# Performance work log

Hardware: AMD Instinct MI355X
Metric: run time of the kernel (lower is better)

Reference implementation:

```python
import jax, jax.numpy as jnp
import numpy as np

B_, DIM, HEADS, RES = 2, 288, 12, 32
# per-branch (D_sp, H_sp, W_sp) from idx permutation of split_size=[2,2,4]
WINS = ((2, 2, 4), (2, 2, 4), (2, 4, 2))
POS_DIM = ((DIM // 3) // 4) // 4  # = 6
HB = HEADS // 3  # heads per branch = 4


def _rel_tables(Dsp, Hsp, Wsp):
    d = np.arange(1 - Dsp, Dsp); h = np.arange(1 - Hsp, Hsp); w = np.arange(1 - Wsp, Wsp)
    biases = np.stack(np.meshgrid(d, h, w, indexing='ij')).reshape(3, -1).T.astype(np.float32)
    c = np.stack(np.meshgrid(np.arange(Dsp), np.arange(Hsp), np.arange(Wsp), indexing='ij')).reshape(3, -1)
    rel = (c[:, :, None] - c[:, None, :]).transpose(1, 2, 0).astype(np.int64)
    rel[..., 0] += Dsp - 1; rel[..., 1] += Hsp - 1; rel[..., 2] += Wsp - 1
    rel[..., 0] *= (2 * Hsp - 1) * (2 * Wsp - 1); rel[..., 1] *= 2 * Wsp - 1
    return biases, rel.sum(-1).astype(np.int32)


def _ln(x, g, b):
    m = x.mean(-1, keepdims=True)
    v = jnp.mean((x - m) ** 2, axis=-1, keepdims=True)
    return (x - m) * jax.lax.rsqrt(v + 1e-5) * g + b


def setup_inputs() -> dict:
    key = jax.random.key(0)
    ks = jax.random.split(key, 10)
    C, P, L = DIM, POS_DIM, RES ** 3
    s = 0.02
    x = jax.random.normal(ks[0], (B_, L, C), jnp.float32)
    w_qkv = jax.random.normal(ks[1], (C, 3 * C), jnp.float32) * s
    w_proj = jax.random.normal(ks[2], (C, C), jnp.float32) * s
    b_proj = jnp.zeros((C,), jnp.float32)
    conv_w = jax.random.normal(ks[3], (C, 1, 3, 3, 3), jnp.float32) * s  # depthwise OIDHW
    conv_b = jnp.zeros((C,), jnp.float32)
    pos_proj_w = jax.random.normal(ks[4], (3, 3, P), jnp.float32) * s
    pos_proj_b = jnp.zeros((3, P), jnp.float32)
    ln1_g = jnp.ones((3, P)); ln1_b = jnp.zeros((3, P))
    lin1_w = jax.random.normal(ks[5], (3, P, P), jnp.float32) * s; lin1_b = jnp.zeros((3, P))
    ln2_g = jnp.ones((3, P)); ln2_b = jnp.zeros((3, P))
    lin2_w = jax.random.normal(ks[6], (3, P, P), jnp.float32) * s; lin2_b = jnp.zeros((3, P))
    ln3_g = jnp.ones((3, P)); ln3_b = jnp.zeros((3, P))
    lin3_w = jax.random.normal(ks[7], (3, P, HB), jnp.float32) * s; lin3_b = jnp.zeros((3, HB))
    tabs = [_rel_tables(*w) for w in WINS]
    rpe_biases = jnp.asarray(np.stack([t[0] for t in tabs]))  # (3, 63, 3)
    rel_index = jnp.asarray(np.stack([t[1] for t in tabs]))   # (3, 16, 16)
    return {'x': x, 'D': RES, 'H': RES, 'W': RES, 'w_qkv': w_qkv, 'w_proj': w_proj,
            'b_proj': b_proj, 'conv_w': conv_w, 'conv_b': conv_b,
            'pos_proj_w': pos_proj_w, 'pos_proj_b': pos_proj_b,
            'ln1_g': ln1_g, 'ln1_b': ln1_b, 'lin1_w': lin1_w, 'lin1_b': lin1_b,
            'ln2_g': ln2_g, 'ln2_b': ln2_b, 'lin2_w': lin2_w, 'lin2_b': lin2_b,
            'ln3_g': ln3_g, 'ln3_b': ln3_b, 'lin3_w': lin3_w, 'lin3_b': lin3_b,
            'rpe_biases': rpe_biases, 'rel_index': rel_index}


def reference(x, D, H, W, w_qkv, w_proj, b_proj, conv_w, conv_b,
              pos_proj_w, pos_proj_b, ln1_g, ln1_b, lin1_w, lin1_b,
              ln2_g, ln2_b, lin2_w, lin2_b, ln3_g, ln3_b, lin3_w, lin3_b,
              rpe_biases, rel_index):
    B, L, C = x.shape
    C3 = C // 3
    hd = C3 // HB
    scale = hd ** -0.5
    qkv = (x @ w_qkv).reshape(B, L, 3, C).transpose(2, 0, 1, 3)  # (3, B, L, C)
    outs = []
    for bi, (Dsp, Hsp, Wsp) in enumerate(WINS):
        N = Dsp * Hsp * Wsp
        lo, hi = bi * C3, (bi + 1) * C3

        def to_win(t):
            # (B, L, C3) -> windows (B', HB, N, hd)
            t = t.reshape(B, D // Dsp, Dsp, H // Hsp, Hsp, W // Wsp, Wsp, C3)
            t = t.transpose(0, 1, 3, 5, 2, 4, 6, 7).reshape(-1, N, HB, hd)
            return t.transpose(0, 2, 1, 3)

        q = to_win(qkv[0, :, :, lo:hi]) * scale
        k = to_win(qkv[1, :, :, lo:hi])
        v = to_win(qkv[2, :, :, lo:hi])
        # dynamic relative position bias MLP (residual=False path)
        p = rpe_biases[bi] @ pos_proj_w[bi] + pos_proj_b[bi]
        p = jax.nn.relu(_ln(p, ln1_g[bi], ln1_b[bi])) @ lin1_w[bi] + lin1_b[bi]
        p = jax.nn.relu(_ln(p, ln2_g[bi], ln2_b[bi])) @ lin2_w[bi] + lin2_b[bi]
        p = jax.nn.relu(_ln(p, ln3_g[bi], ln3_b[bi])) @ lin3_w[bi] + lin3_b[bi]  # (T, HB)
        bias = p[rel_index[bi].reshape(-1)].reshape(N, N, HB).transpose(2, 0, 1)  # (HB, N, N)
        attn = jax.nn.softmax(jnp.einsum('whnd,whmd->whnm', q, k) + bias[None], axis=-1)
        o = jnp.einsum('whnm,whmd->whnd', attn, v)
        o = o.transpose(0, 2, 1, 3).reshape(B, D // Dsp, H // Hsp, W // Wsp, Dsp, Hsp, Wsp, C3)
        o = o.transpose(0, 1, 4, 2, 5, 3, 6, 7).reshape(B, D, H, W, C3)
        outs.append(o)
    att = jnp.concatenate(outs, axis=-1).reshape(B, L, C)
    # locally-enhanced branch: depthwise 3x3x3 conv over v
    vimg = qkv[2].reshape(B, D, H, W, C).transpose(0, 4, 1, 2, 3)
    lcm = jax.lax.conv_general_dilated(vimg, conv_w, (1, 1, 1), 'SAME',
                                       dimension_numbers=('NCDHW', 'OIDHW', 'NCDHW'),
                                       feature_group_count=C)
    lcm = (lcm + conv_b[None, :, None, None, None]).transpose(0, 2, 3, 4, 1).reshape(B, L, C)
    return (att + lcm) @ w_proj + b_proj
```

## Files before the change

### kernel.cpp

```cpp
#include <hip/hip_runtime.h>
#include <hip/hip_bf16.h>
#include <math.h>

#define BATCH 2
#define RES   32
#define LTOK  32768
#define CDIM  288
#define NQKV  864
#define MROWS 65536

typedef unsigned short u16;
typedef u16   u16x4 __attribute__((ext_vector_type(4)));
typedef short s16x8 __attribute__((ext_vector_type(8)));
typedef float f32x4 __attribute__((ext_vector_type(4)));

__device__ __forceinline__ u16 f2bf(float f) {
  union { __hip_bfloat16 h; u16 u; } x;
  x.h = __float2bfloat16(f);
  return x.u;
}
__device__ __forceinline__ float bf2f(u16 u) {
  union { u16 u; __hip_bfloat16 h; } x;
  x.u = u;
  return __bfloat162float(x.h);
}
__device__ __forceinline__ float bflo(unsigned u) {
  union { unsigned u; float f; } x; x.u = u << 16; return x.f;
}
__device__ __forceinline__ float bfhi(unsigned u) {
  union { unsigned u; float f; } x; x.u = u & 0xffff0000u; return x.f;
}

#define ASYNC16(gsrc, ldst)                                                        \
  __builtin_amdgcn_global_load_lds(                                                \
      (const __attribute__((address_space(1))) void*)(gsrc),                       \
      (__attribute__((address_space(3))) void*)(ldst), 16, 0, 0)

__global__ __launch_bounds__(256) void transpose_cvt(
    const float* __restrict__ w, u16* __restrict__ wt, int K, int N) {
  int o = blockIdx.x * 256 + threadIdx.x;
  if (o >= N * K) return;
  int n = o / K, k = o - n * K;
  wt[o] = f2bf(w[(size_t)k * N + n]);
}

__global__ __launch_bounds__(256) void conv_w_kmajor(
    const float* __restrict__ cw, float* __restrict__ wck) {
  int o = blockIdx.x * 256 + threadIdx.x;
  if (o >= 27 * 288) return;
  int k = o / 288, c = o - k * 288;
  wck[o] = cw[c * 27 + k];
}

template <bool BF16OUT, bool ABF16>
__global__ __launch_bounds__(512, 2) void gemm_areg(
    const void* __restrict__ Ax, const u16* __restrict__ Bt,
    const float* __restrict__ bias, void* __restrict__ out, int N) {
  __shared__ __align__(16) u16 lds[36864];
  const int bm = blockIdx.x * 128;
  const int tid = threadIdx.x;
  const int lane = tid & 63, wave = tid >> 6;
  const int m16 = lane & 15, kq = lane >> 4;
  const int nf = wave >> 2, mg = wave & 3;
  const int NC = N >> 5;

  if (ABF16) {
    const u16* Ab = (const u16*)Ax;
    for (int i = wave; i < 72; i += 8) {
      int g = i >> 1, rh = i & 1;
      ASYNC16(Ab + (size_t)(bm + rh * 64 + lane) * 288 + g * 8, &lds[i * 512]);
    }
    asm volatile("s_waitcnt vmcnt(0)" ::: "memory");
  } else {
    const float* Af = (const float*)Ax;
#pragma unroll
    for (int p = 0; p < 18; p++) {
      int s = p * 512 + tid;
      int r = s / 72, q = s - r * 72;
      float4 v = *(const float4*)(Af + (size_t)(bm + r) * 288 + q * 4);
      u16x4 pk;
      pk[0] = f2bf(v.x); pk[1] = f2bf(v.y); pk[2] = f2bf(v.z); pk[3] = f2bf(v.w);
      *(u16x4*)&lds[(q >> 1) * 1024 + (r >> 6) * 512 + (r & 63) * 8 + (q & 1) * 4] = pk;
    }
  }
  __syncthreads();

  s16x8 areg[2][9];
#pragma unroll
  for (int j = 0; j < 2; j++) {
    const int row = (mg * 2 + j) * 16 + m16;
    const int base = (row >> 6) * 512 + (row & 63) * 8;
#pragma unroll
    for (int ks = 0; ks < 9; ks++)
      areg[j][ks] = *(const s16x8*)&lds[(ks * 4 + kq) * 1024 + base];
  }
  asm volatile("s_waitcnt lgkmcnt(0)" ::: "memory");
  __builtin_amdgcn_s_barrier();

  {
    const int r = lane & 31, gh = lane >> 5;
    for (int gp = wave; gp < 18; gp += 8)
      ASYNC16(Bt + (size_t)r * 288 + (gp * 2 + gh) * 8, &lds[gp * 512]);
  }
  asm volatile("s_waitcnt vmcnt(0)" ::: "memory");
  __builtin_amdgcn_s_barrier();

  int buf = 0;
  for (int c = 0; c < NC; c++) {
    if (c + 1 < NC) {
      const u16* Bc = Bt + (size_t)(c + 1) * 32 * 288;
      const int r = lane & 31, gh = lane >> 5;
      u16* bb1 = &lds[(buf ^ 1) * 9216];
      for (int gp = wave; gp < 18; gp += 8)
        ASYNC16(Bc + (size_t)r * 288 + (gp * 2 + gh) * 8, &bb1[gp * 512]);
    }
    __builtin_amdgcn_sched_barrier(0);

    const u16* bb = &lds[buf * 9216];
    f32x4 acc0 = {0.f, 0.f, 0.f, 0.f}, acc1 = {0.f, 0.f, 0.f, 0.f};
#pragma unroll
    for (int ks = 0; ks < 9; ks++) {
      s16x8 bf = *(const s16x8*)&bb[(ks * 4 + kq) * 256 + (nf * 16 + m16) * 8];
      acc0 = __builtin_amdgcn_mfma_f32_16x16x32_bf16(areg[0][ks], bf, acc0, 0, 0, 0);
      acc1 = __builtin_amdgcn_mfma_f32_16x16x32_bf16(areg[1][ks], bf, acc1, 0, 0, 0);
    }
    const int col = (c << 5) + nf * 16 + m16;
    const size_t r0 = (size_t)(bm + mg * 32 + kq * 4);
    if (BF16OUT) {
      u16* op = (u16*)out;
#pragma unroll
      for (int r = 0; r < 4; r++) {
        op[(r0 + r) * N + col] = f2bf(acc0[r]);
        op[(r0 + 16 + r) * N + col] = f2bf(acc1[r]);
      }
    } else {
      const float bv = bias ? bias[col] : 0.f;
      float* op = (float*)out;
#pragma unroll
      for (int r = 0; r < 4; r++) {
        op[(r0 + r) * N + col] = acc0[r] + bv;
        op[(r0 + 16 + r) * N + col] = acc1[r] + bv;
      }
    }
    if (c + 1 < NC) {
      asm volatile("s_waitcnt vmcnt(8)" ::: "memory");
      __builtin_amdgcn_s_barrier();
    }
    buf ^= 1;
  }
}

__device__ __forceinline__ void ln_relu6(const float* x, float* o,
                                         const float* g, const float* b) {
  float m = 0.f;
#pragma unroll
  for (int i = 0; i < 6; i++) m += x[i];
  m *= (1.f / 6.f);
  float v = 0.f;
#pragma unroll
  for (int i = 0; i < 6; i++) { float d = x[i] - m; v += d * d; }
  v *= (1.f / 6.f);
  float r = rsqrtf(v + 1e-5f);
#pragma unroll
  for (int i = 0; i < 6; i++) {
    float t = (x[i] - m) * r * g[i] + b[i];
    o[i] = t > 0.f ? t : 0.f;
  }
}

__global__ __launch_bounds__(256) void rpe_mlp(
    const float* __restrict__ rpe, const float* __restrict__ pw, const float* __restrict__ pb,
    const float* __restrict__ g1, const float* __restrict__ b1,
    const float* __restrict__ w1, const float* __restrict__ bb1,
    const float* __restrict__ g2, const float* __restrict__ b2,
    const float* __restrict__ w2, const float* __restrict__ bb2,
    const float* __restrict__ g3, const float* __restrict__ b3,
    const float* __restrict__ w3, const float* __restrict__ bb3,
    float* __restrict__ ptab) {
  int t = blockIdx.x * blockDim.x + threadIdx.x;
  if (t >= 3 * 63) return;
  int bi = t / 63, row = t % 63;
  float p[6], q[6];
#pragma unroll
  for (int j = 0; j < 6; j++) {
    float s = pb[bi * 6 + j];
#pragma unroll
    for (int i = 0; i < 3; i++) s += rpe[(bi * 63 + row) * 3 + i] * pw[(bi * 3 + i) * 6 + j];
    p[j] = s;
  }
  ln_relu6(p, q, g1 + bi * 6, b1 + bi * 6);
#pragma unroll
  for (int j = 0; j < 6; j++) {
    float s = bb1[bi * 6 + j];
#pragma unroll
    for (int i = 0; i < 6; i++) s += q[i] * w1[(bi * 6 + i) * 6 + j];
    p[j] = s;
  }
  ln_relu6(p, q, g2 + bi * 6, b2 + bi * 6);
#pragma unroll
  for (int j = 0; j < 6; j++) {
    float s = bb2[bi * 6 + j];
#pragma unroll
    for (int i = 0; i < 6; i++) s += q[i] * w2[(bi * 6 + i) * 6 + j];
    p[j] = s;
  }
  ln_relu6(p, q, g3 + bi * 6, b3 + bi * 6);
#pragma unroll
  for (int h = 0; h < 4; h++) {
    float s = bb3[bi * 4 + h];
#pragma unroll
    for (int i = 0; i < 6; i++) s += q[i] * w3[(bi * 6 + i) * 4 + h];
    ptab[(bi * 63 + row) * 4 + h] = s;
  }
}

__global__ __launch_bounds__(256) void attn_kernel(
    const u16* __restrict__ qkv, const float* __restrict__ ptab,
    const int* __restrict__ rel, float* __restrict__ y) {
  __shared__ __align__(16) u16 sq[4][640];
  __shared__ __align__(16) u16 sk[4][640];
  __shared__ __align__(16) u16 svt[4][1280];
  __shared__ __align__(16) u16 sps[4][640];

  const int bi = blockIdx.y;
  const int wsh = (bi == 2) ? 1 : 2;
  const int hsh = (bi == 2) ? 2 : 1;
  const int Wm1 = (1 << wsh) - 1, Hm1 = (1 << hsh) - 1;
  const int nW = RES >> wsh, nH = RES >> hsh;
  const int tid = threadIdx.x;
  const int wv = tid >> 6, lane = tid & 63;
  const int wid = blockIdx.x * 4 + wv;
  const int b = wid >> 11;
  const int r_ = wid & 2047;
  const int w0 = r_ % nW;
  const int r2 = r_ / nW;
  const int h0 = r2 % nH;
  const int d0 = r2 / nH;

  u16* q_  = sq[wv];
  u16* k_  = sk[wv];
  u16* vt_ = svt[wv];
  u16* ps_ = sps[wv];
  const int m16 = lane & 15, q4 = lane >> 4;

  {
    uint4 z = make_uint4(0u, 0u, 0u, 0u);
    if (lane < 16) {
      *(uint4*)&q_[lane * 40 + 24] = z;
      *(uint4*)&k_[lane * 40 + 24] = z;
    }
    if (lane < 40) {
      int row = 24 + lane / 5, ch = (lane % 5) * 8;
      *(uint4*)&vt_[row * 40 + ch] = z;
    }
  }

  int rv[4];
#pragma unroll
  for (int r = 0; r < 4; r++) rv[r] = rel[(bi * 16 + q4 * 4 + r) * 16 + m16];

  size_t ybase[4];
#pragma unroll
  for (int r = 0; r < 4; r++) {
    int n = q4 * 4 + r;
    int dd = n >> 3, hh2 = (n >> wsh) & Hm1, ww = n & Wm1;
    int l = ((d0 * 2 + dd) * RES + ((h0 << hsh) + hh2)) * RES + ((w0 << wsh) + ww);
    ybase[r] = (size_t)(b * LTOK + l) * CDIM + bi * 96;
  }

  const float scale = 0.20412414523193154f;

  for (int hd = 0; hd < 4; hd++) {
    if (lane < 48) {
      int n = lane / 3, ch = (lane % 3) * 8;
      int dd = n >> 3, hh2 = (n >> wsh) & Hm1, ww = n & Wm1;
      int l = ((d0 * 2 + dd) * RES + ((h0 << hsh) + hh2)) * RES + ((w0 << wsh) + ww);
      size_t base = (size_t)(b * LTOK + l) * NQKV + bi * 96 + hd * 24 + ch;
      uint4 qv = *(const uint4*)(qkv + base);
      uint4 kv = *(const uint4*)(qkv + base + 288);
      uint4 vv = *(const uint4*)(qkv + base + 576);
      *(uint4*)&q_[n * 40 + ch] = qv;
      *(uint4*)&k_[n * 40 + ch] = kv;
      const u16* vp = (const u16*)&vv;
#pragma unroll
      for (int j = 0; j < 8; j++) {
        vt_[(ch + j) * 40 + n] = vp[j];
        vt_[(ch + j) * 40 + 16 + n] = vp[j];
      }
    }

    s16x8 af = *(const s16x8*)&q_[m16 * 40 + q4 * 8];
    s16x8 bf = *(const s16x8*)&k_[m16 * 40 + q4 * 8];
    f32x4 sc = __builtin_amdgcn_mfma_f32_16x16x32_bf16(af, bf, (f32x4){0.f, 0.f, 0.f, 0.f}, 0, 0, 0);

    float inv[4];
#pragma unroll
    for (int r = 0; r < 4; r++) {
      float s = sc[r] * scale + ptab[(size_t)(bi * 63 + rv[r]) * 4 + hd];
      float mx = s;
#pragma unroll
      for (int msk = 1; msk <= 8; msk <<= 1) mx = fmaxf(mx, __shfl_xor(mx, msk));
      float e = expf(s - mx);
      float sum = e;
#pragma unroll
      for (int msk = 1; msk <= 8; msk <<= 1) sum += __shfl_xor(sum, msk);
      inv[r] = 1.f / sum;
      u16 hi = f2bf(e);
      float lo = e - bf2f(hi);
      ps_[(q4 * 4 + r) * 40 + m16] = hi;
      ps_[(q4 * 4 + r) * 40 + 16 + m16] = f2bf(lo);
    }

    s16x8 pa = *(const s16x8*)&ps_[m16 * 40 + q4 * 8];
    s16x8 v1 = *(const s16x8*)&vt_[m16 * 40 + q4 * 8];
    s16x8 v2 = *(const s16x8*)&vt_[(16 + m16) * 40 + q4 * 8];
    f32x4 o1 = __builtin_amdgcn_mfma_f32_16x16x32_bf16(pa, v1, (f32x4){0.f, 0.f, 0.f, 0.f}, 0, 0, 0);
    f32x4 o2 = __builtin_amdgcn_mfma_f32_16x16x32_bf16(pa, v2, (f32x4){0.f, 0.f, 0.f, 0.f}, 0, 0, 0);

#pragma unroll
    for (int r = 0; r < 4; r++) {
      float* yp = y + ybase[r] + hd * 24;
      yp[m16] = o1[r] * inv[r];
      if (m16 < 8) yp[16 + m16] = o2[r] * inv[r];
    }
  }
}

template <bool BF16OUT>
__global__ __launch_bounds__(512, 4) void conv_tile_kernel(
    const u16* __restrict__ qkv, const float* __restrict__ wck,
    const float* __restrict__ cb, float* __restrict__ y, u16* __restrict__ ybf) {
  __shared__ __align__(16) u16 vs[1000 * 40];
  const int tid = threadIdx.x;
  const int bx = blockIdx.x;
  const int c0 = blockIdx.y * 32;
  const int b = bx >> 6;
  const int t = bx & 63;
  const int td = (t >> 4) * 8, th = ((t >> 2) & 3) * 8, tw = (t & 3) * 8;

#pragma unroll
  for (int p = 0; p < 8; p++) {
    int idx = p * 512 + tid;
    if (idx < 4000) {
      int tok = idx >> 2, chunk = idx & 3;
      int dz = tok / 100, rem = tok - dz * 100;
      int hz = rem / 10, wz = rem - hz * 10;
      int d = td + dz - 1, h = th + hz - 1, w = tw + wz - 1;
      uint4 v = make_uint4(0u, 0u, 0u, 0u);
      if ((unsigned)d < 32u && (unsigned)h < 32u && (unsigned)w < 32u)
        v = *(const uint4*)(qkv +
              ((size_t)(b * LTOK + ((d * 32 + h) * 32 + w))) * NQKV + 576 + c0 + chunk * 8);
      *(uint4*)&vs[tok * 40 + chunk * 8] = v;
    }
  }
  __syncthreads();

  const int d = tid >> 6, h = (tid >> 3) & 7, w = tid & 7;
  float acc[32];
#pragma unroll
  for (int c = 0; c < 32; c++) acc[c] = cb[c0 + c];

  for (int kd = 0; kd < 3; kd++) {
#pragma unroll
    for (int kh = 0; kh < 3; kh++) {
#pragma unroll
      for (int kw = 0; kw < 3; kw++) {
        const int k = kd * 9 + kh * 3 + kw;
        const float* wk = wck + k * 288 + c0;
        const u16* p0 = &vs[(((d + kd) * 100 + (h + kh) * 10) + (w + kw)) * 40];
#pragma unroll
        for (int cq = 0; cq < 4; cq++) {
          uint4 v0 = *(const uint4*)(p0 + cq * 8);
          const unsigned* u0 = (const unsigned*)&v0;
#pragma unroll
          for (int j = 0; j < 4; j++) {
            const int ce = cq * 8 + j * 2;
            acc[ce]     += bflo(u0[j]) * wk[ce];
            acc[ce + 1] += bfhi(u0[j]) * wk[ce + 1];
          }
        }
      }
    }
  }

  const int tt = b * LTOK + ((td + d) * 32 + (th + h)) * 32 + (tw + w);

  if (BF16OUT) {
    const float4* yp = (const float4*)&y[(size_t)tt * CDIM + c0];
    unsigned pk[16];
#pragma unroll
    for (int q = 0; q < 8; q++) {
      float4 cur = yp[q];
      float va = cur.x + acc[q * 4],     vb = cur.y + acc[q * 4 + 1];
      float vc = cur.z + acc[q * 4 + 2], vd = cur.w + acc[q * 4 + 3];
      pk[q * 2]     = (unsigned)f2bf(va) | ((unsigned)f2bf(vb) << 16);
      pk[q * 2 + 1] = (unsigned)f2bf(vc) | ((unsigned)f2bf(vd) << 16);
    }
    uint4* op = (uint4*)(ybf + (size_t)tt * CDIM + c0);
#pragma unroll
    for (int q = 0; q < 4; q++) op[q] = ((const uint4*)pk)[q];
  } else {
    float4* yp = (float4*)&y[(size_t)tt * CDIM + c0];
#pragma unroll
    for (int q = 0; q < 8; q++) {
      float4 cur = yp[q];
      cur.x += acc[q * 4];     cur.y += acc[q * 4 + 1];
      cur.z += acc[q * 4 + 2]; cur.w += acc[q * 4 + 3];
      yp[q] = cur;
    }
  }
}

extern "C" void kernel_launch(void* const* d_in, const int* in_sizes, int n_in,
                              void* d_out, int out_size, void* d_ws, size_t ws_size,
                              hipStream_t stream) {
  const float* x      = (const float*)d_in[0];
  const float* w_qkv  = (const float*)d_in[4];
  const float* w_proj = (const float*)d_in[5];
  const float* b_proj = (const float*)d_in[6];
  const float* conv_w = (const float*)d_in[7];
  const float* conv_b = (const float*)d_in[8];
  const float* pos_w  = (const float*)d_in[9];
  const float* pos_b  = (const float*)d_in[10];
  const float* ln1_g  = (const float*)d_in[11];
  const float* ln1_b  = (const float*)d_in[12];
  const float* lin1_w = (const float*)d_in[13];
  const float* lin1_b = (const float*)d_in[14];
  const float* ln2_g  = (const float*)d_in[15];
  const float* ln2_b  = (const float*)d_in[16];
  const float* lin2_w = (const float*)d_in[17];
  const float* lin2_b = (const float*)d_in[18];
  const float* ln3_g  = (const float*)d_in[19];
  const float* ln3_b  = (const float*)d_in[20];
  const float* lin3_w = (const float*)d_in[21];
  const float* lin3_b = (const float*)d_in[22];
  const float* rpe    = (const float*)d_in[23];
  const int*   rel    = (const int*)d_in[24];
  float* out = (float*)d_out;

  const size_t Q = (size_t)MROWS * NQKV * sizeof(u16);
  u16* qkv   = (u16*)d_ws;
  u16* wqt   = (u16*)((char*)d_ws + Q);
  u16* wpt   = (u16*)((char*)d_ws + Q + 497664);
  float* ptab  = (float*)((char*)d_ws + Q + 497664 + 165888);
  float* wck   = (float*)((char*)d_ws + Q + 497664 + 165888 + 3024);

  const size_t yoff = (Q + 497664 + 165888 + 3024 + 31104 + 255) & ~(size_t)255;
  const size_t ybf_bytes = (size_t)MROWS * CDIM * sizeof(u16);
  const bool big = ws_size >= yoff + ybf_bytes;
  u16* ybf = (u16*)((char*)d_ws + yoff);

  transpose_cvt<<<(NQKV * CDIM + 255) / 256, 256, 0, stream>>>(w_qkv, wqt, CDIM, NQKV);
  transpose_cvt<<<(CDIM * CDIM + 255) / 256, 256, 0, stream>>>(w_proj, wpt, CDIM, CDIM);
  conv_w_kmajor<<<(27 * 288 + 255) / 256, 256, 0, stream>>>(conv_w, wck);
  gemm_areg<true, false><<<MROWS / 128, 512, 0, stream>>>(x, wqt, nullptr, qkv, NQKV);
  rpe_mlp<<<1, 256, 0, stream>>>(rpe, pos_w, pos_b, ln1_g, ln1_b, lin1_w, lin1_b,
                                 ln2_g, ln2_b, lin2_w, lin2_b, ln3_g, ln3_b,
                                 lin3_w, lin3_b, ptab);
  attn_kernel<<<dim3(1024, 3), 256, 0, stream>>>(qkv, ptab, rel, out);
  if (big) {
    conv_tile_kernel<true><<<dim3(128, 9), 512, 0, stream>>>(qkv, wck, conv_b, out, ybf);
    gemm_areg<false, true><<<MROWS / 128, 512, 0, stream>>>(ybf, wpt, b_proj, out, CDIM);
  } else {
    conv_tile_kernel<false><<<dim3(128, 9), 512, 0, stream>>>(qkv, wck, conv_b, out, nullptr);
    gemm_areg<false, false><<<MROWS / 128, 512, 0, stream>>>(out, wpt, b_proj, out, CDIM);
  }
}
```

Before: 391.8 us.

## Write attention output as bf16, prefetch qkv per head, fold softmax sum into MFMA

```diff
diff --git a/kernel.cpp b/kernel.cpp
--- a/kernel.cpp
+++ b/kernel.cpp
@@ -214,12 +214,13 @@
   }
 }
 
+template <bool BF16OUT>
 __global__ __launch_bounds__(256) void attn_kernel(
     const u16* __restrict__ qkv, const float* __restrict__ ptab,
-    const int* __restrict__ rel, float* __restrict__ y) {
+    const int* __restrict__ rel, float* __restrict__ y, u16* __restrict__ ybf) {
   __shared__ __align__(16) u16 sq[4][640];
   __shared__ __align__(16) u16 sk[4][640];
-  __shared__ __align__(16) u16 svt[4][1280];
+  __shared__ __align__(16) u16 sv[4][640];
   __shared__ __align__(16) u16 sps[4][640];
 
   const int bi = blockIdx.y;
@@ -239,25 +240,23 @@
 
   u16* q_  = sq[wv];
   u16* k_  = sk[wv];
-  u16* vt_ = svt[wv];
+  u16* v_  = sv[wv];
   u16* ps_ = sps[wv];
   const int m16 = lane & 15, q4 = lane >> 4;
 
-  {
+  if (lane < 16) {
     uint4 z = make_uint4(0u, 0u, 0u, 0u);
-    if (lane < 16) {
-      *(uint4*)&q_[lane * 40 + 24] = z;
-      *(uint4*)&k_[lane * 40 + 24] = z;
-    }
-    if (lane < 40) {
-      int row = 24 + lane / 5, ch = (lane % 5) * 8;
-      *(uint4*)&vt_[row * 40 + ch] = z;
-    }
-  }
-
-  int rv[4];
-#pragma unroll
-  for (int r = 0; r < 4; r++) rv[r] = rel[(bi * 16 + q4 * 4 + r) * 16 + m16];
+    *(uint4*)&q_[lane * 40 + 24] = z;
+    *(uint4*)&k_[lane * 40 + 24] = z;
+    *(uint4*)&v_[lane * 40 + 24] = make_uint4(0x3f80u, 0u, 0u, 0u);
+  }
+
+  float4 pt[4];
+#pragma unroll
+  for (int r = 0; r < 4; r++) {
+    int rv = rel[(bi * 16 + q4 * 4 + r) * 16 + m16];
+    pt[r] = *(const float4*)&ptab[(size_t)(bi * 63 + rv) * 4];
+  }
 
   size_t ybase[4];
 #pragma unroll
@@ -268,43 +267,46 @@
     ybase[r] = (size_t)(b * LTOK + l) * CDIM + bi * 96;
   }
 
+  const int sn = lane / 3, sc = (lane % 3) * 8;
+  size_t sbase = 0;
+  if (lane < 48) {
+    int dd = sn >> 3, hh2 = (sn >> wsh) & Hm1, ww = sn & Wm1;
+    int l = ((d0 * 2 + dd) * RES + ((h0 << hsh) + hh2)) * RES + ((w0 << wsh) + ww);
+    sbase = (size_t)(b * LTOK + l) * NQKV + bi * 96 + sc;
+  }
+
   const float scale = 0.20412414523193154f;
 
+  uint4 pq, pk, pv;
+  if (lane < 48) {
+    pq = *(const uint4*)(qkv + sbase);
+    pk = *(const uint4*)(qkv + sbase + 288);
+    pv = *(const uint4*)(qkv + sbase + 576);
+  }
+
+#pragma unroll
   for (int hd = 0; hd < 4; hd++) {
     if (lane < 48) {
-      int n = lane / 3, ch = (lane % 3) * 8;
-      int dd = n >> 3, hh2 = (n >> wsh) & Hm1, ww = n & Wm1;
-      int l = ((d0 * 2 + dd) * RES + ((h0 << hsh) + hh2)) * RES + ((w0 << wsh) + ww);
-      size_t base = (size_t)(b * LTOK + l) * NQKV + bi * 96 + hd * 24 + ch;
-      uint4 qv = *(const uint4*)(qkv + base);
-      uint4 kv = *(const uint4*)(qkv + base + 288);
-      uint4 vv = *(const uint4*)(qkv + base + 576);
-      *(uint4*)&q_[n * 40 + ch] = qv;
-      *(uint4*)&k_[n * 40 + ch] = kv;
-      const u16* vp = (const u16*)&vv;
-#pragma unroll
-      for (int j = 0; j < 8; j++) {
-        vt_[(ch + j) * 40 + n] = vp[j];
-        vt_[(ch + j) * 40 + 16 + n] = vp[j];
-      }
+      *(uint4*)&q_[sn * 40 + sc] = pq;
+      *(uint4*)&k_[sn * 40 + sc] = pk;
+      *(uint4*)&v_[sn * 40 + sc] = pv;
+    }
+    if (hd < 3 && lane < 48) {
+      size_t nb = sbase + (size_t)(hd + 1) * 24;
+      pq = *(const uint4*)(qkv + nb);
+      pk = *(const uint4*)(qkv + nb + 288);
+      pv = *(const uint4*)(qkv + nb + 576);
     }
 
     s16x8 af = *(const s16x8*)&q_[m16 * 40 + q4 * 8];
     s16x8 bf = *(const s16x8*)&k_[m16 * 40 + q4 * 8];
-    f32x4 sc = __builtin_amdgcn_mfma_f32_16x16x32_bf16(af, bf, (f32x4){0.f, 0.f, 0.f, 0.f}, 0, 0, 0);
-
-    float inv[4];
+    f32x4 sc_ = __builtin_amdgcn_mfma_f32_16x16x32_bf16(af, bf, (f32x4){0.f, 0.f, 0.f, 0.f}, 0, 0, 0);
+
 #pragma unroll
     for (int r = 0; r < 4; r++) {
-      float s = sc[r] * scale + ptab[(size_t)(bi * 63 + rv[r]) * 4 + hd];
-      float mx = s;
-#pragma unroll
-      for (int msk = 1; msk <= 8; msk <<= 1) mx = fmaxf(mx, __shfl_xor(mx, msk));
-      float e = expf(s - mx);
-      float sum = e;
-#pragma unroll
-      for (int msk = 1; msk <= 8; msk <<= 1) sum += __shfl_xor(sum, msk);
-      inv[r] = 1.f / sum;
+      const float* ptr4 = (const float*)&pt[r];
+      float s = sc_[r] * scale + ptr4[hd];
+      float e = expf(s);
       u16 hi = f2bf(e);
       float lo = e - bf2f(hi);
       ps_[(q4 * 4 + r) * 40 + m16] = hi;
@@ -312,16 +314,29 @@
     }
 
     s16x8 pa = *(const s16x8*)&ps_[m16 * 40 + q4 * 8];
-    s16x8 v1 = *(const s16x8*)&vt_[m16 * 40 + q4 * 8];
-    s16x8 v2 = *(const s16x8*)&vt_[(16 + m16) * 40 + q4 * 8];
+    s16x8 v1, v2;
+    const int mrow = (q4 & 1) * 8;
+#pragma unroll
+    for (int j = 0; j < 8; j++) {
+      v1[j] = (short)v_[(mrow + j) * 40 + m16];
+      v2[j] = (short)v_[(mrow + j) * 40 + 16 + m16];
+    }
     f32x4 o1 = __builtin_amdgcn_mfma_f32_16x16x32_bf16(pa, v1, (f32x4){0.f, 0.f, 0.f, 0.f}, 0, 0, 0);
     f32x4 o2 = __builtin_amdgcn_mfma_f32_16x16x32_bf16(pa, v2, (f32x4){0.f, 0.f, 0.f, 0.f}, 0, 0, 0);
 
 #pragma unroll
     for (int r = 0; r < 4; r++) {
-      float* yp = y + ybase[r] + hd * 24;
-      yp[m16] = o1[r] * inv[r];
-      if (m16 < 8) yp[16 + m16] = o2[r] * inv[r];
+      float sum = __shfl(o2[r], (lane & 48) + 8);
+      float inv = 1.f / sum;
+      if (BF16OUT) {
+        u16* yp = ybf + ybase[r] + hd * 24;
+        yp[m16] = f2bf(o1[r] * inv);
+        if (m16 < 8) yp[16 + m16] = f2bf(o2[r] * inv);
+      } else {
+        float* yp = y + ybase[r] + hd * 24;
+        yp[m16] = o1[r] * inv;
+        if (m16 < 8) yp[16 + m16] = o2[r] * inv;
+      }
     }
   }
 }
@@ -386,19 +401,21 @@
   const int tt = b * LTOK + ((td + d) * 32 + (th + h)) * 32 + (tw + w);
 
   if (BF16OUT) {
-    const float4* yp = (const float4*)&y[(size_t)tt * CDIM + c0];
-    unsigned pk[16];
-#pragma unroll
-    for (int q = 0; q < 8; q++) {
-      float4 cur = yp[q];
-      float va = cur.x + acc[q * 4],     vb = cur.y + acc[q * 4 + 1];
-      float vc = cur.z + acc[q * 4 + 2], vd = cur.w + acc[q * 4 + 3];
-      pk[q * 2]     = (unsigned)f2bf(va) | ((unsigned)f2bf(vb) << 16);
-      pk[q * 2 + 1] = (unsigned)f2bf(vc) | ((unsigned)f2bf(vd) << 16);
-    }
-    uint4* op = (uint4*)(ybf + (size_t)tt * CDIM + c0);
-#pragma unroll
-    for (int q = 0; q < 4; q++) op[q] = ((const uint4*)pk)[q];
+    uint4* yp = (uint4*)(ybf + (size_t)tt * CDIM + c0);
+#pragma unroll
+    for (int q = 0; q < 4; q++) {
+      uint4 cur = yp[q];
+      unsigned* cu = (unsigned*)&cur;
+      unsigned pk2[4];
+#pragma unroll
+      for (int j = 0; j < 4; j++) {
+        const int ce = q * 8 + j * 2;
+        float a0 = bflo(cu[j]) + acc[ce];
+        float a1 = bfhi(cu[j]) + acc[ce + 1];
+        pk2[j] = (unsigned)f2bf(a0) | ((unsigned)f2bf(a1) << 16);
+      }
+      yp[q] = *(uint4*)pk2;
+    }
   } else {
     float4* yp = (float4*)&y[(size_t)tt * CDIM + c0];
 #pragma unroll
@@ -457,11 +474,12 @@
   rpe_mlp<<<1, 256, 0, stream>>>(rpe, pos_w, pos_b, ln1_g, ln1_b, lin1_w, lin1_b,
                                  ln2_g, ln2_b, lin2_w, lin2_b, ln3_g, ln3_b,
                                  lin3_w, lin3_b, ptab);
-  attn_kernel<<<dim3(1024, 3), 256, 0, stream>>>(qkv, ptab, rel, out);
   if (big) {
-    conv_tile_kernel<true><<<dim3(128, 9), 512, 0, stream>>>(qkv, wck, conv_b, out, ybf);
+    attn_kernel<true><<<dim3(1024, 3), 256, 0, stream>>>(qkv, ptab, rel, nullptr, ybf);
+    conv_tile_kernel<true><<<dim3(128, 9), 512, 0, stream>>>(qkv, wck, conv_b, nullptr, ybf);
     gemm_areg<false, true><<<MROWS / 128, 512, 0, stream>>>(ybf, wpt, b_proj, out, CDIM);
   } else {
+    attn_kernel<false><<<dim3(1024, 3), 256, 0, stream>>>(qkv, ptab, rel, out, nullptr);
     conv_tile_kernel<false><<<dim3(128, 9), 512, 0, stream>>>(qkv, wck, conv_b, out, nullptr);
     gemm_areg<false, false><<<MROWS / 128, 512, 0, stream>>>(out, wpt, b_proj, out, CDIM);
   }
```

Measured after the change: 362.2 us. 7.6% less time.
